# Kernel optimization log

Hardware: AMD Instinct MI355X
Metric: run time of the kernel (lower is better)

The kernel has to match this reference:

```python
import jax, jax.numpy as jnp
import numpy as np

VOCAB, EMB, HID, B, T = 10000, 64, 128, 32, 256


def setup_inputs() -> dict:
    key = jax.random.key(0)
    ks = jax.random.split(key, 5)
    return {
        "inp_ids": jax.random.randint(ks[0], (B, T), 0, VOCAB, dtype=jnp.int64),
        "emb": jax.random.normal(ks[1], (VOCAB, EMB), jnp.float32) * 0.05,
        "W": jax.random.normal(ks[2], (EMB, HID), jnp.float32) * 0.1,
        "U": jax.random.normal(ks[3], (HID, HID), jnp.float32) * 0.1,
        "b": jnp.zeros((HID,), jnp.float32),
        "Wd": jax.random.normal(ks[4], (HID, VOCAB), jnp.float32) * 0.05,
        "bd": jnp.zeros((VOCAB,), jnp.float32),
    }


def reference(inp_ids, emb, W, U, b, Wd, bd):
    # Embedding lookup: [B, T, EMB]
    x = emb[inp_ids]
    # Precompute input contribution for all timesteps: [B, T, HID]
    xw = jnp.einsum("bte,eh->bth", x, W) + b
    # Vanilla RNN scan over time: h_t = tanh(x_t W + b + h_{t-1} U)
    def step(h, xw_t):
        h_new = jnp.tanh(xw_t + h @ U)
        return h_new, h_new

    h0 = jnp.zeros((x.shape[0], U.shape[0]), x.dtype)
    _, hs = jax.lax.scan(step, h0, jnp.swapaxes(xw, 0, 1))  # hs: [T, B, HID]
    rnn_out = jnp.swapaxes(hs, 0, 1)  # [B, T, HID]
    # Output projection to vocab logits: [B, T, VOCAB]
    logits = jnp.einsum("bth,hv->btv", rnn_out, Wd) + bd
    return logits
```

## Files before the change

### kernel.cpp

```cpp
#include <hip/hip_runtime.h>

#define VOCAB 10000
#define EMB 64
#define HID 128
#define BATCH 32
#define TT 256
#define M_TOK (BATCH * TT)
#define NPAD 10112
#define KP 136

typedef float f32x4 __attribute__((ext_vector_type(4)));
typedef float f32x2 __attribute__((ext_vector_type(2)));
typedef short s16x8 __attribute__((ext_vector_type(8)));

__device__ inline unsigned f2bf(float x) {
  unsigned u = __float_as_uint(x);
  return (u + 0x7fffu + ((u >> 16) & 1u)) >> 16;
}

__device__ inline float tanh_fast(float x) {
  float ax = __builtin_fabsf(x);
  float t = __builtin_amdgcn_exp2f(-2.885390082f * ax);
  float r = __builtin_amdgcn_rcpf(1.0f + t);
  float y = (1.0f - t) * r;
  return __builtin_copysignf(y, x);
}

__global__ void k_embed_xw(const int* __restrict__ ids, const float* __restrict__ emb,
                           const float* __restrict__ W, const float* __restrict__ bias,
                           float* __restrict__ xw) {
  __shared__ float er[EMB];
  int tok = blockIdx.x, j = threadIdx.x;
  int id = ids[tok];
  if (j < EMB) er[j] = emb[(long)id * EMB + j];
  __syncthreads();
  float acc = bias[j];
#pragma unroll
  for (int e = 0; e < EMB; ++e) acc = fmaf(er[e], W[e * HID + j], acc);
  xw[tok * HID + j] = acc;
}

__global__ void k_wdt(const float* __restrict__ Wd, ushort* __restrict__ WdT) {
  __shared__ float tile[64][HID + 1];
  int n0 = blockIdx.x * 64;
  int t = threadIdx.x;
  int nn = t & 63, kbase = t >> 6;
#pragma unroll 4
  for (int it = 0; it < 32; ++it) {
    int k = it * 4 + kbase;
    int n = n0 + nn;
    float v = (n < VOCAB) ? Wd[k * VOCAB + n] : 0.0f;
    tile[nn][k] = v;
  }
  __syncthreads();
  int k2 = (t & 63) * 2, row = t >> 6;
#pragma unroll 4
  for (int it = 0; it < 16; ++it) {
    int nn2 = it * 4 + row;
    unsigned pa = f2bf(tile[nn2][k2]);
    unsigned pb = f2bf(tile[nn2][k2 + 1]);
    ((unsigned*)WdT)[(n0 + nn2) * (HID / 2) + (t & 63)] = pa | (pb << 16);
  }
}

__global__ void __launch_bounds__(HID, 1) k_scan(const float* __restrict__ xw,
                                                 const float* __restrict__ U,
                                                 ushort* __restrict__ hout) {
  __shared__ __align__(16) float xs[TT * HID];
  __shared__ __align__(16) float hbuf[2][HID];
  const int b = blockIdx.x, j = threadIdx.x;

  const float* src = xw + (long)b * TT * HID;
#pragma unroll
  for (int it = 0; it < 64; ++it) {
    __builtin_amdgcn_global_load_lds(
        (const __attribute__((address_space(1))) void*)(src + it * 512 + j * 4),
        (__attribute__((address_space(3))) void*)(xs + it * 512 + j * 4),
        16, 0, 0);
  }

  f32x2 u2[64];
#pragma unroll
  for (int i = 0; i < 64; ++i) {
    u2[i].x = U[(2 * i + 0) * HID + j];
    u2[i].y = U[(2 * i + 1) * HID + j];
  }
#pragma unroll
  for (int i = 0; i < 64; ++i) asm volatile("" : "+v"(u2[i]));

  asm volatile("s_waitcnt vmcnt(0) lgkmcnt(0)\n\ts_barrier" ::: "memory");

  ushort* hob = hout + (long)b * TT * HID + j;

  {
    float xv = xs[j];
    float h = tanh_fast(xv);
    hbuf[0][j] = h;
    hob[0] = (ushort)f2bf(h);
  }
  asm volatile("s_waitcnt lgkmcnt(0)\n\ts_barrier" ::: "memory");

  int p = 0;
  for (int t = 1; t < TT; ++t) {
    float xv = xs[t * HID + j];
    f32x2 a0 = {0.f, 0.f}, a1 = {0.f, 0.f}, a2 = {0.f, 0.f}, a3 = {0.f, 0.f};
    const float4* h4 = (const float4*)hbuf[p];
#pragma unroll
    for (int i = 0; i < HID / 8; ++i) {
      float4 hva = h4[2 * i + 0];
      float4 hvb = h4[2 * i + 1];
      f32x2 ha0; ha0.x = hva.x; ha0.y = hva.y;
      f32x2 ha1; ha1.x = hva.z; ha1.y = hva.w;
      f32x2 hb0; hb0.x = hvb.x; hb0.y = hvb.y;
      f32x2 hb1; hb1.x = hvb.z; hb1.y = hvb.w;
      a0 += ha0 * u2[4 * i + 0];
      a1 += ha1 * u2[4 * i + 1];
      a2 += hb0 * u2[4 * i + 2];
      a3 += hb1 * u2[4 * i + 3];
    }
    f32x2 s2 = (a0 + a1) + (a2 + a3);
    float h = tanh_fast(s2.x + s2.y + xv);
    hbuf[1 - p][j] = h;
    hob[t * HID] = (ushort)f2bf(h);
    p ^= 1;
    asm volatile("s_waitcnt lgkmcnt(0)\n\ts_barrier" ::: "memory");
  }
}

__global__ void __launch_bounds__(256, 2) k_gemm(const ushort* __restrict__ A,
                                                 const ushort* __restrict__ Bt,
                                                 const float* __restrict__ bd,
                                                 float* __restrict__ out) {
  __shared__ ushort As[128 * KP];
  __shared__ ushort Bs[128 * KP];
  int m0 = blockIdx.x * 128, n0 = blockIdx.y * 128;
  int t = threadIdx.x;
#pragma unroll
  for (int it = 0; it < 8; ++it) {
    int c = it * 256 + t;
    int row = c >> 4, off = c & 15;
    uint4 va = ((const uint4*)(A + (m0 + row) * HID))[off];
    *((uint4*)(As + row * KP + off * 8)) = va;
    uint4 vb = ((const uint4*)(Bt + (n0 + row) * HID))[off];
    *((uint4*)(Bs + row * KP + off * 8)) = vb;
  }
  __syncthreads();

  int lane = t & 63, w = t >> 6;
  int wm = (w >> 1) * 64, wn = (w & 1) * 64;
  int fm = lane & 15, kq = lane >> 4;

  f32x4 acc[4][4];
#pragma unroll
  for (int mt = 0; mt < 4; ++mt)
#pragma unroll
    for (int nt = 0; nt < 4; ++nt) acc[mt][nt] = (f32x4){0.f, 0.f, 0.f, 0.f};

#pragma unroll
  for (int ks = 0; ks < 4; ++ks) {
    s16x8 af[4], bf[4];
#pragma unroll
    for (int mt = 0; mt < 4; ++mt)
      af[mt] = *(const s16x8*)(As + (wm + mt * 16 + fm) * KP + ks * 32 + kq * 8);
#pragma unroll
    for (int nt = 0; nt < 4; ++nt)
      bf[nt] = *(const s16x8*)(Bs + (wn + nt * 16 + fm) * KP + ks * 32 + kq * 8);
#pragma unroll
    for (int mt = 0; mt < 4; ++mt)
#pragma unroll
      for (int nt = 0; nt < 4; ++nt)
        acc[mt][nt] = __builtin_amdgcn_mfma_f32_16x16x32_bf16(af[mt], bf[nt], acc[mt][nt], 0, 0, 0);
  }

#pragma unroll
  for (int mt = 0; mt < 4; ++mt) {
    int rbase = m0 + wm + mt * 16 + kq * 4;
#pragma unroll
    for (int nt = 0; nt < 4; ++nt) {
      int col = n0 + wn + nt * 16 + fm;
      if (col < VOCAB) {
        float bdv = bd[col];
#pragma unroll
        for (int r = 0; r < 4; ++r)
          out[(long)(rbase + r) * VOCAB + col] = acc[mt][nt][r] + bdv;
      }
    }
  }
}

extern "C" void kernel_launch(void* const* d_in, const int* in_sizes, int n_in,
                              void* d_out, int out_size, void* d_ws, size_t ws_size,
                              hipStream_t stream) {
  const int* ids = (const int*)d_in[0];
  const float* emb = (const float*)d_in[1];
  const float* W = (const float*)d_in[2];
  const float* U = (const float*)d_in[3];
  const float* b = (const float*)d_in[4];
  const float* Wd = (const float*)d_in[5];
  const float* bd = (const float*)d_in[6];
  float* out = (float*)d_out;

  char* ws = (char*)d_ws;
  float* xw = (float*)ws;
  ushort* hbf = (ushort*)(ws + 4u * 1024 * 1024);
  ushort* wdt = (ushort*)(ws + 6u * 1024 * 1024);

  k_embed_xw<<<dim3(M_TOK), dim3(HID), 0, stream>>>(ids, emb, W, b, xw);
  k_wdt<<<dim3(NPAD / 64), dim3(256), 0, stream>>>(Wd, wdt);
  k_scan<<<dim3(BATCH), dim3(HID), 0, stream>>>(xw, U, hbf);
  k_gemm<<<dim3(M_TOK / 128, NPAD / 128), dim3(256), 0, stream>>>(hbf, wdt, bd, out);
}
```

Baseline: 512.8 us.

## Run RNN scan with a single wavefront per batch to drop barriers

The recurrent scan kernel now uses one 64-lane wavefront per batch row instead of two, with each lane computing two hidden units. Half of U is held in VGPRs and the other half is pinned to AGPRs. Because only one wavefront shares the LDS state, the per-timestep s_barrier is removed and only an LDS waitcnt remains. The cost is twice the FMA work per lane on the serial critical path, plus possible AGPR-to-VGPR moves to read the U values held in AGPRs.

Result: slower. 727.9 us (+41.9%).

```diff
diff --git a/kernel.cpp b/kernel.cpp
--- a/kernel.cpp
+++ b/kernel.cpp
@@ -63,47 +63,55 @@
   }
 }
 
-__global__ void __launch_bounds__(HID, 1) k_scan(const float* __restrict__ xw,
-                                                 const float* __restrict__ U,
-                                                 ushort* __restrict__ hout) {
+__global__ void __launch_bounds__(64, 1) k_scan(const float* __restrict__ xw,
+                                                const float* __restrict__ U,
+                                                ushort* __restrict__ hout) {
   __shared__ __align__(16) float xs[TT * HID];
   __shared__ __align__(16) float hbuf[2][HID];
-  const int b = blockIdx.x, j = threadIdx.x;
+  const int b = blockIdx.x, l = threadIdx.x;
 
   const float* src = xw + (long)b * TT * HID;
 #pragma unroll
-  for (int it = 0; it < 64; ++it) {
+  for (int it = 0; it < 128; ++it) {
     __builtin_amdgcn_global_load_lds(
-        (const __attribute__((address_space(1))) void*)(src + it * 512 + j * 4),
-        (__attribute__((address_space(3))) void*)(xs + it * 512 + j * 4),
+        (const __attribute__((address_space(1))) void*)(src + it * 256 + l * 4),
+        (__attribute__((address_space(3))) void*)(xs + it * 256 + l * 4),
         16, 0, 0);
   }
 
-  f32x2 u2[64];
+  f32x2 u0[64], u1[64];
 #pragma unroll
   for (int i = 0; i < 64; ++i) {
-    u2[i].x = U[(2 * i + 0) * HID + j];
-    u2[i].y = U[(2 * i + 1) * HID + j];
-  }
-#pragma unroll
-  for (int i = 0; i < 64; ++i) asm volatile("" : "+v"(u2[i]));
-
-  asm volatile("s_waitcnt vmcnt(0) lgkmcnt(0)\n\ts_barrier" ::: "memory");
-
-  ushort* hob = hout + (long)b * TT * HID + j;
+    u0[i].x = U[(2 * i + 0) * HID + l];
+    u0[i].y = U[(2 * i + 1) * HID + l];
+    u1[i].x = U[(2 * i + 0) * HID + 64 + l];
+    u1[i].y = U[(2 * i + 1) * HID + 64 + l];
+  }
+#pragma unroll
+  for (int i = 0; i < 64; ++i) asm volatile("" : "+v"(u0[i]));
+#pragma unroll
+  for (int i = 0; i < 64; ++i) asm volatile("" : "+a"(u1[i]));
+
+  asm volatile("s_waitcnt vmcnt(0) lgkmcnt(0)" ::: "memory");
+
+  ushort* hob = hout + (long)b * TT * HID + l;
 
   {
-    float xv = xs[j];
-    float h = tanh_fast(xv);
-    hbuf[0][j] = h;
-    hob[0] = (ushort)f2bf(h);
-  }
-  asm volatile("s_waitcnt lgkmcnt(0)\n\ts_barrier" ::: "memory");
+    float h0 = tanh_fast(xs[l]);
+    float h1 = tanh_fast(xs[64 + l]);
+    hbuf[0][l] = h0;
+    hbuf[0][64 + l] = h1;
+    hob[0] = (ushort)f2bf(h0);
+    hob[64] = (ushort)f2bf(h1);
+  }
+  asm volatile("s_waitcnt lgkmcnt(0)" ::: "memory");
 
   int p = 0;
   for (int t = 1; t < TT; ++t) {
-    float xv = xs[t * HID + j];
+    float xv0 = xs[t * HID + l];
+    float xv1 = xs[t * HID + 64 + l];
     f32x2 a0 = {0.f, 0.f}, a1 = {0.f, 0.f}, a2 = {0.f, 0.f}, a3 = {0.f, 0.f};
+    f32x2 c0 = {0.f, 0.f}, c1 = {0.f, 0.f}, c2 = {0.f, 0.f}, c3 = {0.f, 0.f};
     const float4* h4 = (const float4*)hbuf[p];
 #pragma unroll
     for (int i = 0; i < HID / 8; ++i) {
@@ -113,17 +121,25 @@
       f32x2 ha1; ha1.x = hva.z; ha1.y = hva.w;
       f32x2 hb0; hb0.x = hvb.x; hb0.y = hvb.y;
       f32x2 hb1; hb1.x = hvb.z; hb1.y = hvb.w;
-      a0 += ha0 * u2[4 * i + 0];
-      a1 += ha1 * u2[4 * i + 1];
-      a2 += hb0 * u2[4 * i + 2];
-      a3 += hb1 * u2[4 * i + 3];
+      a0 += ha0 * u0[4 * i + 0];
+      a1 += ha1 * u0[4 * i + 1];
+      a2 += hb0 * u0[4 * i + 2];
+      a3 += hb1 * u0[4 * i + 3];
+      c0 += ha0 * u1[4 * i + 0];
+      c1 += ha1 * u1[4 * i + 1];
+      c2 += hb0 * u1[4 * i + 2];
+      c3 += hb1 * u1[4 * i + 3];
     }
     f32x2 s2 = (a0 + a1) + (a2 + a3);
-    float h = tanh_fast(s2.x + s2.y + xv);
-    hbuf[1 - p][j] = h;
-    hob[t * HID] = (ushort)f2bf(h);
+    f32x2 s3 = (c0 + c1) + (c2 + c3);
+    float h0 = tanh_fast(s2.x + s2.y + xv0);
+    float h1 = tanh_fast(s3.x + s3.y + xv1);
+    hbuf[1 - p][l] = h0;
+    hbuf[1 - p][64 + l] = h1;
+    hob[t * HID] = (ushort)f2bf(h0);
+    hob[t * HID + 64] = (ushort)f2bf(h1);
     p ^= 1;
-    asm volatile("s_waitcnt lgkmcnt(0)\n\ts_barrier" ::: "memory");
+    asm volatile("s_waitcnt lgkmcnt(0)" ::: "memory");
   }
 }
 
@@ -207,6 +223,6 @@
 
   k_embed_xw<<<dim3(M_TOK), dim3(HID), 0, stream>>>(ids, emb, W, b, xw);
   k_wdt<<<dim3(NPAD / 64), dim3(256), 0, stream>>>(Wd, wdt);
-  k_scan<<<dim3(BATCH), dim3(HID), 0, stream>>>(xw, U, hbf);
+  k_scan<<<dim3(BATCH), dim3(64), 0, stream>>>(xw, U, hbf);
   k_gemm<<<dim3(M_TOK / 128, NPAD / 128), dim3(256), 0, stream>>>(hbf, wdt, bd, out);
 }
```
